# Kernel optimization log

Measured on AMD Instinct MI355X. Metric: run time of the kernel, lower is better.

Reference implementation:

```python
import jax, jax.numpy as jnp
import numpy as np

B = 2_000_000
EPS = 1e-7


def _skew(v):
    # v: [..., 3] -> [..., 3, 3] skew-symmetric
    z = jnp.zeros_like(v[..., 0])
    return jnp.stack([
        jnp.stack([z, -v[..., 2], v[..., 1]], axis=-1),
        jnp.stack([v[..., 2], z, -v[..., 0]], axis=-1),
        jnp.stack([-v[..., 1], v[..., 0], z], axis=-1),
    ], axis=-2)


def _rodrigues(phi):
    # axis-angle [..., 3] -> rotation matrix [..., 3, 3]
    angle = jnp.linalg.norm(phi, axis=-1, keepdims=True)
    axis = phi / jnp.maximum(angle, 1e-12)
    K = _skew(axis)
    a = angle[..., None]
    I = jnp.eye(3, dtype=phi.dtype)
    return I + jnp.sin(a) * K + (1.0 - jnp.cos(a)) * (K @ K)


def setup_inputs() -> dict:
    key = jax.random.key(0)
    k1, k2, k3 = jax.random.split(key, 3)
    # random rotations via exp-map of random axis-angle vectors
    phi_est = jax.random.normal(k1, (B, 3), dtype=jnp.float32) * 0.8
    phi_tgt = jax.random.normal(k2, (B, 3), dtype=jnp.float32) * 0.8
    C_est = _rodrigues(phi_est)
    C_target = _rodrigues(phi_tgt)
    # SPD information matrices: A A^T + I  (logdet well-defined)
    A = 0.3 * jax.random.normal(k3, (B, 3, 3), dtype=jnp.float32)
    Rinv = jnp.einsum('bij,bkj->bik', A, A) + jnp.eye(3, dtype=jnp.float32)
    return {"C_est": C_est, "C_target": C_target, "Rinv": Rinv}


def so3_log(C):
    # batched SO(3) log map -> [..., 3]
    tr = C[..., 0, 0] + C[..., 1, 1] + C[..., 2, 2]
    cos_angle = jnp.clip(0.5 * (tr - 1.0), -1.0 + EPS, 1.0 - EPS)
    angle = jnp.arccos(cos_angle)
    sin_angle = jnp.sin(angle)
    # angle/(2 sin angle); small-angle Taylor: 0.5 + angle^2/12
    small = angle < 1e-6
    coef = jnp.where(small, 0.5 + angle * angle / 12.0,
                     0.5 * angle / jnp.where(small, 1.0, sin_angle))
    skew = C - jnp.swapaxes(C, -1, -2)
    vee = jnp.stack([skew[..., 2, 1], skew[..., 0, 2], skew[..., 1, 0]], axis=-1)
    return coef[..., None] * vee


def batch_logdet3(M):
    det = (M[..., 0, 0] * (M[..., 1, 1] * M[..., 2, 2] - M[..., 1, 2] * M[..., 2, 1])
           - M[..., 0, 1] * (M[..., 1, 0] * M[..., 2, 2] - M[..., 1, 2] * M[..., 2, 0])
           + M[..., 0, 2] * (M[..., 1, 0] * M[..., 2, 1] - M[..., 1, 1] * M[..., 2, 0]))
    return jnp.log(det)


def reference(C_est, C_target, Rinv):
    # residual = log(C_est @ C_target^T)  -> [B, 3]
    dC = jnp.einsum('bij,bkj->bik', C_est, C_target)
    residual = so3_log(dC)
    # 0.5 * r^T Rinv r  -> [B]
    weighted = 0.5 * jnp.einsum('bi,bij,bj->b', residual, Rinv, residual)
    nll = weighted - 0.5 * batch_logdet3(Rinv)
    return nll
```

## Files before the change

### kernel.cpp

```cpp
#include <hip/hip_runtime.h>

constexpr int BLK = 256;

__device__ __forceinline__ float mul_rn(float a, float b) {
    float r; asm("v_mul_f32 %0, %1, %2" : "=v"(r) : "v"(a), "v"(b)); return r;
}
__device__ __forceinline__ float add_rn(float a, float b) {
    float r; asm("v_add_f32 %0, %1, %2" : "=v"(r) : "v"(a), "v"(b)); return r;
}
__device__ __forceinline__ float sub_rn(float a, float b) {
    float r; asm("v_sub_f32 %0, %1, %2" : "=v"(r) : "v"(a), "v"(b)); return r;
}
__device__ __forceinline__ float fma_rn(float a, float b, float c) {
    float r; asm("v_fma_f32 %0, %1, %2, %3"
                 : "=v"(r) : "v"(a), "v"(b), "v"(c)); return r;
}

__device__ __forceinline__ float dot3_fma_asc(float a0, float a1, float a2,
                                              float b0, float b1, float b2) {
    return fma_rn(a2, b2, fma_rn(a1, b1, mul_rn(a0, b0)));
}

__global__ __launch_bounds__(BLK, 8) void so3_nll_kernel(
    const float* __restrict__ C_est,
    const float* __restrict__ C_tgt,
    const float* __restrict__ Rinv,
    float* __restrict__ out,
    int B)
{
    __shared__ float sE[BLK * 9];
    __shared__ float sT[BLK * 9];

    const int tid  = threadIdx.x;
    const int b0   = blockIdx.x * BLK;
    const int nrem = min(BLK, B - b0);
    const int nflt = nrem * 9;
    const int nvec = nflt >> 2;

    const float4* gE = reinterpret_cast<const float4*>(C_est + (size_t)b0 * 9);
    const float4* gT = reinterpret_cast<const float4*>(C_tgt + (size_t)b0 * 9);

    for (int i = tid; i < nvec; i += BLK) {
        float4 e = gE[i];
        float4 t = gT[i];
        *reinterpret_cast<float4*>(&sE[i * 4]) = e;
        *reinterpret_cast<float4*>(&sT[i * 4]) = t;
    }
    for (int i = (nvec << 2) + tid; i < nflt; i += BLK) {
        sE[i] = C_est[(size_t)b0 * 9 + i];
        sT[i] = C_tgt[(size_t)b0 * 9 + i];
    }

    float R0 = 0.f, R1 = 0.f, R2 = 0.f, R3 = 0.f, R4 = 0.f,
          R5 = 0.f, R6 = 0.f, R7 = 0.f, R8 = 0.f;
    if (tid < nrem) {
        const float* Rp = Rinv + (size_t)(b0 + tid) * 9;
        R0 = Rp[0]; R1 = Rp[1]; R2 = Rp[2];
        R3 = Rp[3]; R4 = Rp[4]; R5 = Rp[5];
        R6 = Rp[6]; R7 = Rp[7]; R8 = Rp[8];
    }

    __syncthreads();

    if (tid < nrem) {
        const float* E = &sE[tid * 9];
        const float* T = &sT[tid * 9];

        float d00 = dot3_fma_asc(E[0],E[1],E[2], T[0],T[1],T[2]);
        float d11 = dot3_fma_asc(E[3],E[4],E[5], T[3],T[4],T[5]);
        float d22 = dot3_fma_asc(E[6],E[7],E[8], T[6],T[7],T[8]);

        float tr = add_rn(add_rn(d00, d11), d22);
        float ca = 0.5f * sub_rn(tr, 1.0f);
        constexpr float HI = 1.0f - 1e-7f;
        ca = fminf(fmaxf(ca, -HI), HI);
        float angle = acosf(ca);
        float sa    = sinf(angle);
        float coef = (0.5f * angle) / sa;

        float d01 = dot3_fma_asc(E[0],E[1],E[2], T[3],T[4],T[5]);
        float d02 = dot3_fma_asc(E[0],E[1],E[2], T[6],T[7],T[8]);
        float d10 = dot3_fma_asc(E[3],E[4],E[5], T[0],T[1],T[2]);
        float d12 = dot3_fma_asc(E[3],E[4],E[5], T[6],T[7],T[8]);
        float d20 = dot3_fma_asc(E[6],E[7],E[8], T[0],T[1],T[2]);
        float d21 = dot3_fma_asc(E[6],E[7],E[8], T[3],T[4],T[5]);

        float r0 = coef * sub_rn(d21, d12);
        float r1 = coef * sub_rn(d02, d20);
        float r2 = coef * sub_rn(d10, d01);

        float w = 0.5f * (r0 * ((R0*r0 + R1*r1) + R2*r2) +
                          r1 * ((R3*r0 + R4*r1) + R5*r2) +
                          r2 * ((R6*r0 + R7*r1) + R8*r2));

        float det = R0 * (R4*R8 - R5*R7)
                  - R1 * (R3*R8 - R5*R6)
                  + R2 * (R3*R7 - R4*R6);

        out[b0 + tid] = w - 0.5f * logf(det);
    }
}

extern "C" void kernel_launch(void* const* d_in, const int* in_sizes, int n_in,
                              void* d_out, int out_size, void* d_ws, size_t ws_size,
                              hipStream_t stream) {
    const float* C_est = (const float*)d_in[0];
    const float* C_tgt = (const float*)d_in[1];
    const float* Rinv  = (const float*)d_in[2];
    float* out = (float*)d_out;

    const int B = in_sizes[0] / 9;
    const int blocks = (B + BLK - 1) / BLK;
    so3_nll_kernel<<<blocks, BLK, 0, stream>>>(C_est, C_tgt, Rinv, out, B);
}
```

Baseline: 207.9 us.

## Convert to persistent grid with double-buffered LDS prefetch of next chunk

The one-block-per-chunk launch becomes a grid-stride persistent kernel capped at 1024 blocks. Each block double-buffers the rotation matrices in shared memory: it loads the next chunk's float4 data into registers, computes the current chunk, then writes the prefetched data to the other LDS buffer. The goal is to overlap global load latency with compute and to cut block launch overhead. In exchange, shared memory per block doubles, launch bounds drop to 4 blocks per CU, and the capped grid may undersubscribe the GPU for a memory-bound kernel.

```diff
diff --git a/kernel.cpp b/kernel.cpp
--- a/kernel.cpp
+++ b/kernel.cpp
@@ -1,6 +1,7 @@
 #include <hip/hip_runtime.h>
 
 constexpr int BLK = 256;
+constexpr int GRID_CAP = 1024;
 
 __device__ __forceinline__ float mul_rn(float a, float b) {
     float r; asm("v_mul_f32 %0, %1, %2" : "=v"(r) : "v"(a), "v"(b)); return r;
@@ -21,83 +22,131 @@
     return fma_rn(a2, b2, fma_rn(a1, b1, mul_rn(a0, b0)));
 }
 
-__global__ __launch_bounds__(BLK, 8) void so3_nll_kernel(
+__global__ __launch_bounds__(BLK, 4) void so3_nll_kernel(
     const float* __restrict__ C_est,
     const float* __restrict__ C_tgt,
     const float* __restrict__ Rinv,
     float* __restrict__ out,
     int B)
 {
-    __shared__ float sE[BLK * 9];
-    __shared__ float sT[BLK * 9];
+    __shared__ float sE[2][BLK * 9];
+    __shared__ float sT[2][BLK * 9];
 
-    const int tid  = threadIdx.x;
-    const int b0   = blockIdx.x * BLK;
-    const int nrem = min(BLK, B - b0);
-    const int nflt = nrem * 9;
-    const int nvec = nflt >> 2;
+    const int tid     = threadIdx.x;
+    const int nchunks = (B + BLK - 1) / BLK;
+    const int G       = gridDim.x;
 
-    const float4* gE = reinterpret_cast<const float4*>(C_est + (size_t)b0 * 9);
-    const float4* gT = reinterpret_cast<const float4*>(C_tgt + (size_t)b0 * 9);
+    int c = blockIdx.x;
+    if (c >= nchunks) return;
 
-    for (int i = tid; i < nvec; i += BLK) {
-        float4 e = gE[i];
-        float4 t = gT[i];
-        *reinterpret_cast<float4*>(&sE[i * 4]) = e;
-        *reinterpret_cast<float4*>(&sT[i * 4]) = t;
+    {
+        const int b0   = c * BLK;
+        const int nflt = min(BLK, B - b0) * 9;
+        const int nvec = nflt >> 2;
+        const float4* gE = reinterpret_cast<const float4*>(C_est + (size_t)b0 * 9);
+        const float4* gT = reinterpret_cast<const float4*>(C_tgt + (size_t)b0 * 9);
+        for (int i = tid; i < nvec; i += BLK) {
+            float4 e = gE[i];
+            float4 t = gT[i];
+            *reinterpret_cast<float4*>(&sE[0][i * 4]) = e;
+            *reinterpret_cast<float4*>(&sT[0][i * 4]) = t;
+        }
+        for (int i = (nvec << 2) + tid; i < nflt; i += BLK) {
+            sE[0][i] = C_est[(size_t)b0 * 9 + i];
+            sT[0][i] = C_tgt[(size_t)b0 * 9 + i];
+        }
     }
-    for (int i = (nvec << 2) + tid; i < nflt; i += BLK) {
-        sE[i] = C_est[(size_t)b0 * 9 + i];
-        sT[i] = C_tgt[(size_t)b0 * 9 + i];
-    }
-
-    float R0 = 0.f, R1 = 0.f, R2 = 0.f, R3 = 0.f, R4 = 0.f,
-          R5 = 0.f, R6 = 0.f, R7 = 0.f, R8 = 0.f;
-    if (tid < nrem) {
-        const float* Rp = Rinv + (size_t)(b0 + tid) * 9;
-        R0 = Rp[0]; R1 = Rp[1]; R2 = Rp[2];
-        R3 = Rp[3]; R4 = Rp[4]; R5 = Rp[5];
-        R6 = Rp[6]; R7 = Rp[7]; R8 = Rp[8];
-    }
-
     __syncthreads();
 
-    if (tid < nrem) {
-        const float* E = &sE[tid * 9];
-        const float* T = &sT[tid * 9];
+    int cur = 0;
+    for (; c < nchunks; c += G) {
+        const int b0   = c * BLK;
+        const int nrem = min(BLK, B - b0);
 
-        float d00 = dot3_fma_asc(E[0],E[1],E[2], T[0],T[1],T[2]);
-        float d11 = dot3_fma_asc(E[3],E[4],E[5], T[3],T[4],T[5]);
-        float d22 = dot3_fma_asc(E[6],E[7],E[8], T[6],T[7],T[8]);
+        const float* Rp = Rinv + (size_t)(b0 + min(tid, nrem - 1)) * 9;
+        float R0 = Rp[0], R1 = Rp[1], R2 = Rp[2];
+        float R3 = Rp[3], R4 = Rp[4], R5 = Rp[5];
+        float R6 = Rp[6], R7 = Rp[7], R8 = Rp[8];
 
-        float tr = add_rn(add_rn(d00, d11), d22);
-        float ca = 0.5f * sub_rn(tr, 1.0f);
-        constexpr float HI = 1.0f - 1e-7f;
-        ca = fminf(fmaxf(ca, -HI), HI);
-        float angle = acosf(ca);
-        float sa    = sinf(angle);
-        float coef = (0.5f * angle) / sa;
+        const int  cn       = c + G;
+        const bool has_next = (cn < nchunks);
+        float4 eA, eB, eC, tA, tB, tC;
+        float  scE = 0.f, scT = 0.f;
+        int    nvecN = 0, nfltN = 0, tiN = 0;
+        if (has_next) {
+            const int b0n = cn * BLK;
+            nfltN = min(BLK, B - b0n) * 9;
+            nvecN = nfltN >> 2;
+            const float4* gEn = reinterpret_cast<const float4*>(C_est + (size_t)b0n * 9);
+            const float4* gTn = reinterpret_cast<const float4*>(C_tgt + (size_t)b0n * 9);
+            const int iA = min(tid,           nvecN - 1);
+            const int iB = min(tid + BLK,     nvecN - 1);
+            const int iC = min(tid + 2 * BLK, nvecN - 1);
+            eA = gEn[iA]; tA = gTn[iA];
+            eB = gEn[iB]; tB = gTn[iB];
+            eC = gEn[iC]; tC = gTn[iC];
+            tiN = (nvecN << 2) + tid;
+            if (tiN < nfltN) {
+                scE = C_est[(size_t)b0n * 9 + tiN];
+                scT = C_tgt[(size_t)b0n * 9 + tiN];
+            }
+        }
 
-        float d01 = dot3_fma_asc(E[0],E[1],E[2], T[3],T[4],T[5]);
-        float d02 = dot3_fma_asc(E[0],E[1],E[2], T[6],T[7],T[8]);
-        float d10 = dot3_fma_asc(E[3],E[4],E[5], T[0],T[1],T[2]);
-        float d12 = dot3_fma_asc(E[3],E[4],E[5], T[6],T[7],T[8]);
-        float d20 = dot3_fma_asc(E[6],E[7],E[8], T[0],T[1],T[2]);
-        float d21 = dot3_fma_asc(E[6],E[7],E[8], T[3],T[4],T[5]);
+        if (tid < nrem) {
+            const float* E = &sE[cur][tid * 9];
+            const float* T = &sT[cur][tid * 9];
 
-        float r0 = coef * sub_rn(d21, d12);
-        float r1 = coef * sub_rn(d02, d20);
-        float r2 = coef * sub_rn(d10, d01);
+            float d00 = dot3_fma_asc(E[0],E[1],E[2], T[0],T[1],T[2]);
+            float d11 = dot3_fma_asc(E[3],E[4],E[5], T[3],T[4],T[5]);
+            float d22 = dot3_fma_asc(E[6],E[7],E[8], T[6],T[7],T[8]);
 
-        float w = 0.5f * (r0 * ((R0*r0 + R1*r1) + R2*r2) +
-                          r1 * ((R3*r0 + R4*r1) + R5*r2) +
-                          r2 * ((R6*r0 + R7*r1) + R8*r2));
+            float tr = add_rn(add_rn(d00, d11), d22);
+            float ca = 0.5f * sub_rn(tr, 1.0f);
+            constexpr float HI = 1.0f - 1e-7f;
+            ca = fminf(fmaxf(ca, -HI), HI);
+            float angle = acosf(ca);
+            float sa    = sinf(angle);
+            float coef = (0.5f * angle) / sa;
 
-        float det = R0 * (R4*R8 - R5*R7)
-                  - R1 * (R3*R8 - R5*R6)
-                  + R2 * (R3*R7 - R4*R6);
+            float d01 = dot3_fma_asc(E[0],E[1],E[2], T[3],T[4],T[5]);
+            float d02 = dot3_fma_asc(E[0],E[1],E[2], T[6],T[7],T[8]);
+            float d10 = dot3_fma_asc(E[3],E[4],E[5], T[0],T[1],T[2]);
+            float d12 = dot3_fma_asc(E[3],E[4],E[5], T[6],T[7],T[8]);
+            float d20 = dot3_fma_asc(E[6],E[7],E[8], T[0],T[1],T[2]);
+            float d21 = dot3_fma_asc(E[6],E[7],E[8], T[3],T[4],T[5]);
 
-        out[b0 + tid] = w - 0.5f * logf(det);
+            float r0 = coef * sub_rn(d21, d12);
+            float r1 = coef * sub_rn(d02, d20);
+            float r2 = coef * sub_rn(d10, d01);
+
+            float w = 0.5f * (r0 * ((R0*r0 + R1*r1) + R2*r2) +
+                              r1 * ((R3*r0 + R4*r1) + R5*r2) +
+                              r2 * ((R6*r0 + R7*r1) + R8*r2));
+
+            float det = R0 * (R4*R8 - R5*R7)
+                      - R1 * (R3*R8 - R5*R6)
+                      + R2 * (R3*R7 - R4*R6);
+
+            out[b0 + tid] = w - 0.5f * logf(det);
+        }
+
+        if (has_next) {
+            float* dE = sE[cur ^ 1];
+            float* dT = sT[cur ^ 1];
+            const int iA = min(tid,           nvecN - 1);
+            const int iB = min(tid + BLK,     nvecN - 1);
+            const int iC = min(tid + 2 * BLK, nvecN - 1);
+            *reinterpret_cast<float4*>(&dE[iA * 4]) = eA;
+            *reinterpret_cast<float4*>(&dT[iA * 4]) = tA;
+            *reinterpret_cast<float4*>(&dE[iB * 4]) = eB;
+            *reinterpret_cast<float4*>(&dT[iB * 4]) = tB;
+            *reinterpret_cast<float4*>(&dE[iC * 4]) = eC;
+            *reinterpret_cast<float4*>(&dT[iC * 4]) = tC;
+            if (tiN < nfltN) { dE[tiN] = scE; dT[tiN] = scT; }
+        }
+
+        __syncthreads();
+        cur ^= 1;
     }
 }
 
@@ -110,6 +159,7 @@
     float* out = (float*)d_out;
 
     const int B = in_sizes[0] / 9;
-    const int blocks = (B + BLK - 1) / BLK;
+    const int nchunks = (B + BLK - 1) / BLK;
+    const int blocks = nchunks < GRID_CAP ? nchunks : GRID_CAP;
     so3_nll_kernel<<<blocks, BLK, 0, stream>>>(C_est, C_tgt, Rinv, out, B);
 }
```

Result: no change. 207.7 us (-0.1%).
